# Kernel optimization log

Measured on AMD Instinct MI355X. Metric: run time of the kernel, lower is better.

Reference implementation:

```python
import jax, jax.numpy as jnp
import numpy as np

B, SWIN_D, VIT_D, E, H = 16384, 768, 512, 1024, 4
HD = E // H  # 256


def setup_inputs() -> dict:
    key = jax.random.key(0)
    ks = jax.random.split(key, 12)
    s = lambda fan_in: 1.0 / np.sqrt(fan_in)
    return {
        "swin_feat": jax.random.normal(ks[0], (B, SWIN_D), jnp.float32),
        "vit_feat": jax.random.normal(ks[1], (B, VIT_D), jnp.float32),
        # outer projections (nn.Linear: y = x @ W.T + b)
        "Wq": jax.random.uniform(ks[2], (E, SWIN_D), jnp.float32, -s(SWIN_D), s(SWIN_D)),
        "bq": jax.random.uniform(ks[3], (E,), jnp.float32, -s(SWIN_D), s(SWIN_D)),
        "Wk": jax.random.uniform(ks[4], (E, VIT_D), jnp.float32, -s(VIT_D), s(VIT_D)),
        "bk": jax.random.uniform(ks[5], (E,), jnp.float32, -s(VIT_D), s(VIT_D)),
        "Wv": jax.random.uniform(ks[6], (E, VIT_D), jnp.float32, -s(VIT_D), s(VIT_D)),
        "bv": jax.random.uniform(ks[7], (E,), jnp.float32, -s(VIT_D), s(VIT_D)),
        # nn.MultiheadAttention internal in_proj (stacked q,k,v) and out_proj
        "in_proj_w": jax.random.uniform(ks[8], (3 * E, E), jnp.float32, -s(E), s(E)),
        "in_proj_b": jnp.zeros((3 * E,), jnp.float32),
        "Wo": jax.random.uniform(ks[9], (E, E), jnp.float32, -s(E), s(E)),
        "bo": jnp.zeros((E,), jnp.float32),
    }


def reference(swin_feat, vit_feat, Wq, bq, Wk, bk, Wv, bv, in_proj_w, in_proj_b, Wo, bo):
    # outer projections -> [B, E] (seq_len = 1, so the seq dim is implicit)
    q = swin_feat @ Wq.T + bq
    k = vit_feat @ Wk.T + bk
    v = vit_feat @ Wv.T + bv
    # MultiheadAttention in-projection (split stacked weight)
    Wiq, Wik, Wiv = in_proj_w[:E], in_proj_w[E:2 * E], in_proj_w[2 * E:]
    biq, bik, biv = in_proj_b[:E], in_proj_b[E:2 * E], in_proj_b[2 * E:]
    q2 = (q @ Wiq.T + biq).reshape(B, H, HD)
    k2 = (k @ Wik.T + bik).reshape(B, H, HD)
    v2 = (v @ Wiv.T + biv).reshape(B, H, HD)
    # attention with q_len = kv_len = 1
    scale = 1.0 / np.sqrt(HD)
    scores = jnp.einsum('bhd,bhd->bh', q2, k2) * scale        # [B, H]
    w = jax.nn.softmax(scores[..., None], axis=-1)             # softmax over 1 key -> ones
    attn = w * v2                                              # [B, H, HD]
    out = attn.reshape(B, E) @ Wo.T + bo                       # out-projection
    return out
```

## Files before the change

### kernel.cpp

```cpp
#include <hip/hip_runtime.h>
#include <stdint.h>
#include <stddef.h>

#define E_DIM 1024

typedef __bf16 v8bf __attribute__((ext_vector_type(8)));
typedef float v4f __attribute__((ext_vector_type(4)));

__device__ __forceinline__ unsigned short f2bf(float x) {
  unsigned int u = __builtin_bit_cast(unsigned int, x);
  u += 0x7fffu + ((u >> 16) & 1u);
  return (unsigned short)(u >> 16);
}

template <int RB>
__device__ __forceinline__ int swz(int r, int c) {
  if constexpr (RB >= 128) return c ^ ((r & 7) << 4);
  else return c;
}

template <int N>
__device__ __forceinline__ void waitcnt_vm() {
  static_assert(N == 0 || N == 4 || N == 8 || N == 12, "add literal");
  if constexpr (N == 0)  asm volatile("s_waitcnt vmcnt(0)" ::: "memory");
  if constexpr (N == 4)  asm volatile("s_waitcnt vmcnt(4)" ::: "memory");
  if constexpr (N == 8)  asm volatile("s_waitcnt vmcnt(8)" ::: "memory");
  if constexpr (N == 12) asm volatile("s_waitcnt vmcnt(12)" ::: "memory");
}

template <int ROWS, int BK>
__device__ __forceinline__ void stageg(const unsigned short* __restrict__ G, int g0,
                                       int ldg, int k0, char* L, int wid, int lane) {
  constexpr int RB = BK * 2;
  constexpr int ITERS = (ROWS * RB) / 4096;
#pragma unroll
  for (int it = 0; it < ITERS; ++it) {
    int lbase = it * 4096 + wid * 1024;
    int lin = lbase + lane * 16;
    int r = lin / RB, cb = lin % RB;
    int gcb = swz<RB>(r, cb);
    const char* g = (const char*)G + ((size_t)(g0 + r) * ldg + k0) * 2 + gcb;
    __builtin_amdgcn_global_load_lds((const __attribute__((address_space(1))) void*)g,
                                     (__attribute__((address_space(3))) void*)(L + lbase),
                                     16, 0, 0);
  }
}

template <int RB>
__device__ __forceinline__ v8bf frag_bf16(const char* L, int r, int kelem) {
  int o = swz<RB>(r, kelem * 2);
  return *(const v8bf*)(L + r * RB + o);
}

template <int BM, int BN, int BK, int FM, int FN>
__device__ __forceinline__ void compute_tile(const char* Al, const char* Bl,
                                             v4f (&acc)[FM][FN],
                                             int wr, int wc, int lr, int kg) {
  constexpr int RBA = BK * 2, RBB = BK * 2;
  constexpr int TMW = BM / 2, TNW = BN / 2;
#pragma unroll
  for (int kk = 0; kk < BK / 32; ++kk) {
    const int ke = kk * 32 + kg * 8;
    v8bf a[FM], b[FN];
#pragma unroll
    for (int mi = 0; mi < FM; ++mi)
      a[mi] = frag_bf16<RBA>(Al, wr * TMW + mi * 16 + lr, ke);
#pragma unroll
    for (int ni = 0; ni < FN; ++ni)
      b[ni] = frag_bf16<RBB>(Bl, wc * TNW + ni * 16 + lr, ke);
#pragma unroll
    for (int mi = 0; mi < FM; ++mi)
#pragma unroll
      for (int ni = 0; ni < FN; ++ni)
        acc[mi][ni] = __builtin_amdgcn_mfma_f32_16x16x32_bf16(a[mi], b[ni], acc[mi][ni], 0, 0, 0);
  }
}

__device__ __forceinline__ void cvt4(const float4* __restrict__ src,
                                     ushort4* __restrict__ dst, int i0) {
#pragma unroll
  for (int j = 0; j < 4; ++j) {
    int i = i0 + j * 256;
    float4 f = src[i];
    ushort4 u;
    u.x = f2bf(f.x); u.y = f2bf(f.y); u.z = f2bf(f.z); u.w = f2bf(f.w);
    dst[i] = u;
  }
}

__device__ __forceinline__ void mv4(const float* __restrict__ W, const float* __restrict__ x,
                                    const float* __restrict__ b, float* __restrict__ y,
                                    int blkrel, int tid) {
  int r = blkrel * 4 + (tid >> 6);
  int lane = tid & 63;
  float s = 0.f;
  for (int c = lane; c < 1024; c += 64) s += W[(size_t)r * 1024 + c] * x[c];
#pragma unroll
  for (int off = 32; off; off >>= 1) s += __shfl_down(s, off);
  if (lane == 0) y[r] = s + b[r];
}

__global__ __launch_bounds__(256) void prep1(const float* __restrict__ Wv,
                                             unsigned short* __restrict__ WvT,
                                             const float* __restrict__ Wiv,
                                             const float* __restrict__ bv,
                                             const float* __restrict__ biv,
                                             float* __restrict__ b1,
                                             unsigned short* __restrict__ Wivb) {
  int bid = blockIdx.x;
  int tid = threadIdx.x;
  if (bid < 512) {
    __shared__ float tile[32][33];
    const int R = 1024, C = 512;
    int nbx = C >> 5;
    int bx = bid % nbx, by = bid / nbx;
    int tx = tid & 31, ty = tid >> 5;
#pragma unroll
    for (int i = 0; i < 32; i += 8)
      tile[ty + i][tx] = Wv[(size_t)(by * 32 + ty + i) * C + bx * 32 + tx];
    __syncthreads();
#pragma unroll
    for (int i = 0; i < 32; i += 8)
      WvT[(size_t)(bx * 32 + ty + i) * R + by * 32 + tx] = f2bf(tile[tx][ty + i]);
  } else if (bid < 768) {
    mv4(Wiv, bv, biv, b1, bid - 512, tid);
  } else {
    cvt4((const float4*)Wiv, (ushort4*)Wivb, (bid - 768) * 1024 + tid);
  }
}

template <int BM, int BN, int BK, int FM, int FN, int OUTBF, int XCDSWZ>
__global__ __launch_bounds__(256) void gemm_cv(const unsigned short* __restrict__ A,
                                               const unsigned short* __restrict__ B,
                                               const float* __restrict__ bias,
                                               float* __restrict__ Cf,
                                               unsigned short* __restrict__ Cb,
                                               int M, int N, int K,
                                               const float* __restrict__ mvW,
                                               const float* __restrict__ mvx,
                                               const float* __restrict__ mvb,
                                               float* __restrict__ mvy, int nmv,
                                               const float* __restrict__ csrc1,
                                               unsigned short* __restrict__ cdst1,
                                               int cbase1, int ncv1,
                                               const float* __restrict__ csrc2,
                                               unsigned short* __restrict__ cdst2,
                                               int cbase2) {
  static_assert((BM + BN) * BK * 2 / 1024 / 4 == 4, "vmcnt literals assume 4 loads/tile/wave");
  __shared__ __align__(16) char Al0[BM * BK * 2];
  __shared__ __align__(16) char Al1[BM * BK * 2];
  __shared__ __align__(16) char Al2[BM * BK * 2];
  __shared__ __align__(16) char Al3[BM * BK * 2];
  __shared__ __align__(16) char Bl0[BN * BK * 2];
  __shared__ __align__(16) char Bl1[BN * BK * 2];
  __shared__ __align__(16) char Bl2[BN * BK * 2];
  __shared__ __align__(16) char Bl3[BN * BK * 2];
  const int nbn = N / BN;
  const int ngemm = nbn * (M / BM);
  int bid = blockIdx.x;
  const int tid = threadIdx.x;

  if (bid >= ngemm) {
    int rel = bid - ngemm;
    if (rel < nmv) {
      mv4(mvW, mvx, mvb, mvy, rel, tid);
    } else if (rel < nmv + ncv1) {
      cvt4((const float4*)csrc1, (ushort4*)cdst1, (cbase1 + rel - nmv) * 1024 + tid);
    } else {
      cvt4((const float4*)csrc2, (ushort4*)cdst2, (cbase2 + rel - nmv - ncv1) * 1024 + tid);
    }
    return;
  }

  int bm_i, bn_i;
  if (XCDSWZ) {
    int x = bid & 7, j = bid >> 3;
    bm_i = x + ((j >> 3) << 3);
    bn_i = j & 7;
  } else {
    bm_i = bid / nbn;
    bn_i = bid % nbn;
  }
  const int bm0 = bm_i * BM, bn0 = bn_i * BN;

  constexpr int TMW = BM / 2, TNW = BN / 2;
  const int lane = tid & 63;
  const int wid = tid >> 6;
  const int wr = wid >> 1, wc = wid & 1;
  const int lr = lane & 15;
  const int kg = lane >> 4;

  v4f acc[FM][FN];
#pragma unroll
  for (int i = 0; i < FM; ++i)
#pragma unroll
    for (int j = 0; j < FN; ++j) acc[i][j] = 0.f;

  const int NT = K / BK;

  stageg<BM, BK>(A, bm0, K, 0 * BK, Al0, wid, lane);
  stageg<BN, BK>(B, bn0, K, 0 * BK, Bl0, wid, lane);
  stageg<BM, BK>(A, bm0, K, 1 * BK, Al1, wid, lane);
  stageg<BN, BK>(B, bn0, K, 1 * BK, Bl1, wid, lane);
  stageg<BM, BK>(A, bm0, K, 2 * BK, Al2, wid, lane);
  stageg<BN, BK>(B, bn0, K, 2 * BK, Bl2, wid, lane);
  stageg<BM, BK>(A, bm0, K, 3 * BK, Al3, wid, lane);
  stageg<BN, BK>(B, bn0, K, 3 * BK, Bl3, wid, lane);

#define GEMM_PHASE(AB, BB, TNXT, W)                                      \
  waitcnt_vm<W>();                                                       \
  __builtin_amdgcn_s_barrier();                                          \
  __builtin_amdgcn_sched_barrier(0);                                     \
  compute_tile<BM, BN, BK, FM, FN>(AB, BB, acc, wr, wc, lr, kg);         \
  __builtin_amdgcn_sched_barrier(0);                                     \
  asm volatile("s_waitcnt lgkmcnt(0)" ::: "memory");                     \
  __builtin_amdgcn_s_barrier();                                          \
  if ((TNXT) < NT) {                                                     \
    stageg<BM, BK>(A, bm0, K, (TNXT)*BK, AB, wid, lane);                 \
    stageg<BN, BK>(B, bn0, K, (TNXT)*BK, BB, wid, lane);                 \
  }

  for (int t = 0; t < NT - 4; t += 4) {
    GEMM_PHASE(Al0, Bl0, t + 4, 12)
    GEMM_PHASE(Al1, Bl1, t + 5, 12)
    GEMM_PHASE(Al2, Bl2, t + 6, 12)
    GEMM_PHASE(Al3, Bl3, t + 7, 12)
  }
  GEMM_PHASE(Al0, Bl0, NT, 12)
  GEMM_PHASE(Al1, Bl1, NT, 8)
  GEMM_PHASE(Al2, Bl2, NT, 4)
  GEMM_PHASE(Al3, Bl3, NT, 0)
#undef GEMM_PHASE

#pragma unroll
  for (int ni = 0; ni < FN; ++ni) {
    int col = bn0 + wc * TNW + ni * 16 + lr;
    float bz = bias ? bias[col] : 0.f;
#pragma unroll
    for (int mi = 0; mi < FM; ++mi) {
      int row0 = bm0 + wr * TMW + mi * 16 + kg * 4;
#pragma unroll
      for (int r = 0; r < 4; ++r) {
        float v = acc[mi][ni][r] + bz;
        if (OUTBF) Cb[(size_t)(row0 + r) * N + col] = f2bf(v);
        else       Cf[(size_t)(row0 + r) * N + col] = v;
      }
    }
  }
}

extern "C" void kernel_launch(void* const* d_in, const int* in_sizes, int n_in,
                              void* d_out, int out_size, void* d_ws, size_t ws_size,
                              hipStream_t stream) {
  const float* vit = (const float*)d_in[1];
  const float* Wv  = (const float*)d_in[6];
  const float* bv  = (const float*)d_in[7];
  const float* ipw = (const float*)d_in[8];
  const float* ipb = (const float*)d_in[9];
  const float* Wo  = (const float*)d_in[10];
  const float* bo  = (const float*)d_in[11];
  const float* Wiv = ipw + 2 * E_DIM * E_DIM;
  const float* biv = ipb + 2 * E_DIM;

  char* ws = (char*)d_ws;
  unsigned short* Xb   = (unsigned short*)(ws);
  unsigned short* Wivb = (unsigned short*)(ws + (16 << 20));
  unsigned short* Wob  = (unsigned short*)(ws + (18 << 20));
  unsigned short* WvTb = (unsigned short*)(ws + (20 << 20));
  unsigned short* Ttb  = (unsigned short*)(ws + (21 << 20));
  unsigned short* Wcb  = (unsigned short*)(ws + (22 << 20));
  float* b1 = (float*)(ws + (23 << 20));
  float* bc = (float*)(ws + (23 << 20) + 4096);

  prep1<<<1024, 256, 0, stream>>>(Wv, WvTb, Wiv, bv, biv, b1, Wivb);

  gemm_cv<64, 64, 64, 2, 2, 1, 0><<<128 + 256 + 256 + 1024, 256, 0, stream>>>(
      WvTb, Wivb, nullptr, nullptr, Ttb, 512, 1024, 1024,
      Wo, b1, bo, bc, 256,
      Wo, Wob, 0, 256,
      vit, Xb, 0);

  gemm_cv<64, 64, 64, 2, 2, 1, 0><<<128 + 1024, 256, 0, stream>>>(
      Wob, Ttb, nullptr, nullptr, Wcb, 1024, 512, 1024,
      nullptr, nullptr, nullptr, nullptr, 0,
      vit, Xb, 1024, 1024,
      vit, Xb, 0);

  gemm_cv<128, 128, 32, 4, 4, 0, 1><<<1024, 256, 0, stream>>>(
      Xb, Wcb, bc, (float*)d_out, nullptr, 16384, 1024, 512,
      nullptr, nullptr, nullptr, nullptr, 0,
      nullptr, nullptr, 0, 0,
      nullptr, nullptr, 0);
}
```

Before: 59.94 us.

## Restructure GEMM pipeline to single barrier per tile with 3-deep prefetch

```diff
diff --git a/kernel.cpp b/kernel.cpp
--- a/kernel.cpp
+++ b/kernel.cpp
@@ -204,32 +204,30 @@
   stageg<BN, BK>(B, bn0, K, 1 * BK, Bl1, wid, lane);
   stageg<BM, BK>(A, bm0, K, 2 * BK, Al2, wid, lane);
   stageg<BN, BK>(B, bn0, K, 2 * BK, Bl2, wid, lane);
-  stageg<BM, BK>(A, bm0, K, 3 * BK, Al3, wid, lane);
-  stageg<BN, BK>(B, bn0, K, 3 * BK, Bl3, wid, lane);
-
-#define GEMM_PHASE(AB, BB, TNXT, W)                                      \
+
+#define GEMM_PHASE(CA, CB, SA, SB, TNXT, W)                              \
   waitcnt_vm<W>();                                                       \
   __builtin_amdgcn_s_barrier();                                          \
   __builtin_amdgcn_sched_barrier(0);                                     \
-  compute_tile<BM, BN, BK, FM, FN>(AB, BB, acc, wr, wc, lr, kg);         \
-  __builtin_amdgcn_sched_barrier(0);                                     \
-  asm volatile("s_waitcnt lgkmcnt(0)" ::: "memory");                     \
-  __builtin_amdgcn_s_barrier();                                          \
   if ((TNXT) < NT) {                                                     \
-    stageg<BM, BK>(A, bm0, K, (TNXT)*BK, AB, wid, lane);                 \
-    stageg<BN, BK>(B, bn0, K, (TNXT)*BK, BB, wid, lane);                 \
-  }
-
-  for (int t = 0; t < NT - 4; t += 4) {
-    GEMM_PHASE(Al0, Bl0, t + 4, 12)
-    GEMM_PHASE(Al1, Bl1, t + 5, 12)
-    GEMM_PHASE(Al2, Bl2, t + 6, 12)
-    GEMM_PHASE(Al3, Bl3, t + 7, 12)
-  }
-  GEMM_PHASE(Al0, Bl0, NT, 12)
-  GEMM_PHASE(Al1, Bl1, NT, 8)
-  GEMM_PHASE(Al2, Bl2, NT, 4)
-  GEMM_PHASE(Al3, Bl3, NT, 0)
+    stageg<BM, BK>(A, bm0, K, (TNXT)*BK, SA, wid, lane);                 \
+    stageg<BN, BK>(B, bn0, K, (TNXT)*BK, SB, wid, lane);                 \
+  }                                                                      \
+  __builtin_amdgcn_s_setprio(1);                                         \
+  compute_tile<BM, BN, BK, FM, FN>(CA, CB, acc, wr, wc, lr, kg);         \
+  __builtin_amdgcn_s_setprio(0);                                         \
+  __builtin_amdgcn_sched_barrier(0);
+
+  for (int t = 0; t + 8 <= NT; t += 4) {
+    GEMM_PHASE(Al0, Bl0, Al3, Bl3, t + 3, 8)
+    GEMM_PHASE(Al1, Bl1, Al0, Bl0, t + 4, 8)
+    GEMM_PHASE(Al2, Bl2, Al1, Bl1, t + 5, 8)
+    GEMM_PHASE(Al3, Bl3, Al2, Bl2, t + 6, 8)
+  }
+  GEMM_PHASE(Al0, Bl0, Al3, Bl3, NT - 1, 8)
+  GEMM_PHASE(Al1, Bl1, Al0, Bl0, NT, 8)
+  GEMM_PHASE(Al2, Bl2, Al1, Bl1, NT, 4)
+  GEMM_PHASE(Al3, Bl3, Al2, Bl2, NT, 0)
 #undef GEMM_PHASE
 
 #pragma unroll
```

Result: no change. 59.00 us (-1.6%).
